# Optimization experiments

Measured on AMD Instinct MI355X. Metric: run time of the kernel, lower is better.

The kernel has to match this reference:

```python
import jax, jax.numpy as jnp
import numpy as np

VOCAB = 100
EMB = 256
HID = 256
B = 8
S = 2048


def setup_inputs() -> dict:
    key = jax.random.key(0)
    ks = jax.random.split(key, 12)
    s_e = 1.0 / np.sqrt(EMB)
    s_h = 1.0 / np.sqrt(HID)
    return {
        "x": jax.random.randint(ks[0], (B, S), 0, VOCAB),
        "embedding": jax.random.normal(ks[1], (VOCAB, EMB), jnp.float32),
        "w_ih": jax.random.uniform(ks[2], (3 * HID, EMB), jnp.float32, -s_e, s_e),
        "w_hh": jax.random.uniform(ks[3], (3 * HID, HID), jnp.float32, -s_h, s_h),
        "b_ih": jax.random.uniform(ks[4], (3 * HID,), jnp.float32, -s_h, s_h),
        "b_hh": jax.random.uniform(ks[5], (3 * HID,), jnp.float32, -s_h, s_h),
        "attn_w": jax.random.uniform(ks[6], (HID, HID), jnp.float32, -s_h, s_h),
        "attn_b": jax.random.uniform(ks[7], (HID,), jnp.float32, -s_h, s_h),
        "comb_w": jax.random.uniform(ks[8], (HID, 2 * HID), jnp.float32, -s_h, s_h),
        "comb_b": jax.random.uniform(ks[9], (HID,), jnp.float32, -s_h, s_h),
        "fc_w": jax.random.uniform(ks[10], (VOCAB, HID), jnp.float32, -s_h, s_h),
        "fc_b": jax.random.uniform(ks[11], (VOCAB,), jnp.float32, -s_h, s_h),
    }


def _gru(emb, w_ih, w_hh, b_ih, b_hh):
    # emb: [B, S, E]; PyTorch GRU gate order: r, z, n
    xg = jnp.einsum('bse,ge->bsg', emb, w_ih) + b_ih  # [B, S, 3H]
    h0 = jnp.zeros((emb.shape[0], HID), emb.dtype)

    def step(h, xg_t):
        hg = h @ w_hh.T + b_hh
        xr, xz, xn = jnp.split(xg_t, 3, axis=-1)
        hr, hz, hn = jnp.split(hg, 3, axis=-1)
        r = jax.nn.sigmoid(xr + hr)
        z = jax.nn.sigmoid(xz + hz)
        n = jnp.tanh(xn + r * hn)
        h_new = (1.0 - z) * n + z * h
        return h_new, h_new

    h_last, hs = jax.lax.scan(step, h0, jnp.swapaxes(xg, 0, 1))
    return jnp.swapaxes(hs, 0, 1), h_last  # [B,S,H], [B,H]


def reference(x, embedding, w_ih, w_hh, b_ih, b_hh, attn_w, attn_b, comb_w, comb_b, fc_w, fc_b):
    emb = embedding[x]  # [B, S, E]
    all_h, h_last = _gru(emb, w_ih, w_hh, b_ih, b_hh)
    keys = jnp.einsum('bsh,kh->bsk', all_h, attn_w) + attn_b  # [B,S,H]
    scores = jnp.einsum('bqh,bkh->bqk', all_h, keys)  # [B,S,S]
    seq = all_h.shape[1]
    causal = jnp.tril(jnp.ones((seq, seq), bool))
    scores = jnp.where(causal[None], scores, -jnp.inf)
    attn = jax.nn.softmax(scores, axis=-1)
    context = jnp.einsum('bqk,bkh->bqh', attn, all_h)  # [B,S,H]
    combined = jnp.concatenate([all_h, context], axis=-1)
    combined = jnp.tanh(jnp.einsum('bsd,hd->bsh', combined, comb_w) + comb_b)
    output = jnp.einsum('bsh,vh->bsv', combined, fc_w) + fc_b
    return output, h_last[None]  # hidden: [num_layers=1, B, H]
```

## Files before the change

kernel.cpp:

```cpp
#include <hip/hip_runtime.h>

#define SEQ  2048
#define NB   8
#define HD   256
#define G3   768
#define NV   100
#define KVB  32

typedef float f32x4 __attribute__((ext_vector_type(4)));
typedef int   i32x4 __attribute__((ext_vector_type(4)));
typedef short s16x8 __attribute__((ext_vector_type(8)));
typedef unsigned short u16x4 __attribute__((ext_vector_type(4)));

#define INV26 1.490116119384765625e-8f

__device__ __forceinline__ float rcp_fast(float x) {
  return __builtin_amdgcn_rcpf(x);
}
__device__ __forceinline__ float sigm(float x) {
  x = fminf(fmaxf(x, -30.f), 30.f);
  return rcp_fast(1.f + __expf(-x));
}
__device__ __forceinline__ float tanh_fast(float x) {
  x = fminf(fmaxf(x, -15.f), 15.f);
  float e = __expf(2.f * x);
  return (e - 1.f) * rcp_fast(e + 1.f);
}
__device__ __forceinline__ void cvt_hilo(float f, unsigned short& h, unsigned short& l) {
  unsigned u = __float_as_uint(f);
  h = (unsigned short)(u >> 16);
  float r = f - __uint_as_float(u & 0xffff0000u);
  l = (unsigned short)(__float_as_uint(r) >> 16);
}

__global__ __launch_bounds__(256) void build_table(
    const float* __restrict__ emb, const float* __restrict__ w_ih,
    const float* __restrict__ b_ih, float* __restrict__ table) {
  __shared__ float eL[256];
  __shared__ float wL[256][37];
  int v = blockIdx.x, tid = threadIdx.x;
  eL[tid] = emb[v * HD + tid];
  for (int gt = 0; gt < 3; ++gt) {
    float acc = b_ih[gt * 256 + tid];
    for (int e0 = 0; e0 < HD; e0 += 32) {
      __syncthreads();
      #pragma unroll
      for (int i = 0; i < 32; ++i) {
        int idx = tid + i * 256;
        int r = idx >> 5, c = idx & 31;
        wL[r][c] = w_ih[(size_t)(gt * 256 + r) * HD + e0 + c];
      }
      __syncthreads();
      #pragma unroll
      for (int c = 0; c < 32; ++c) acc += eL[e0 + c] * wL[tid][c];
    }
    table[((size_t)v * 256 + tid) * 4 + gt] = acc;
  }
}

__global__ void __launch_bounds__(512) gru_scan(
    const int* __restrict__ x, const float* __restrict__ w_hh,
    const float* __restrict__ b_hh, const float* __restrict__ table,
    float* __restrict__ all_h, float* __restrict__ h_last) {
  __shared__ __align__(16) signed char hpk[2][2 * 272];
  __shared__ int xs[SEQ];
  const int b = blockIdx.x;
  int tid = threadIdx.x;
  int lane = tid & 63, wv = tid >> 6;
  int ncol = lane & 15, quad = lane >> 4;
  int usel = quad & 1;
  int j = wv * 32 + usel * 16 + ncol;

  for (int i = tid; i < SEQ; i += 512) xs[i] = x[b * SEQ + i];
  for (int i = tid; i < 2 * 272; i += 512)
    hpk[0][i] = (i >= 272) ? (signed char)-128 : 0;

  i32x4 bw[2][3][4];
  float Cn2[2][3];
  #pragma unroll
  for (int u = 0; u < 2; ++u) {
    #pragma unroll
    for (int t3 = 0; t3 < 3; ++t3) {
      int row = t3 * 256 + wv * 32 + u * 16 + ncol;
      int sw = 0;
      #pragma unroll
      for (int c = 0; c < 4; ++c) {
        const float* p = w_hh + (size_t)row * HD + c * 64 + quad * 16;
        unsigned pw[4] = {0u, 0u, 0u, 0u};
        #pragma unroll
        for (int e = 0; e < 16; ++e) {
          int q = __float2int_rn(p[e] * 2048.f);
          q = max(-127, min(127, q));
          sw += q;
          pw[e >> 2] |= ((unsigned)(q & 255)) << ((e & 3) * 8);
        }
        bw[u][t3][c] = (i32x4){(int)pw[0], (int)pw[1], (int)pw[2], (int)pw[3]};
      }
      sw += __shfl_xor(sw, 16);
      sw += __shfl_xor(sw, 32);
      Cn2[u][t3] = b_hh[row] + 128.f * (float)sw * INV26;
    }
  }
  float Csel[3];
  #pragma unroll
  for (int t3 = 0; t3 < 3; ++t3) Csel[t3] = usel ? Cn2[1][t3] : Cn2[0][t3];

  float hreg = 0.f;
  __syncthreads();
  float xr, xz, xn;
  {
    int v = xs[0];
    f32x4 xg = *(const f32x4*)&table[((size_t)v * 256 + j) * 4];
    xr = xg[0]; xz = xg[1]; xn = xg[2];
  }
  int a_base = (ncol & 1) * 272 + quad * 16;

  for (int t = 0; t < SEQ; ++t) {
    const signed char* cb = hpk[t & 1];
    i32x4 a[4];
    #pragma unroll
    for (int c = 0; c < 4; ++c)
      a[c] = *(const i32x4*)&cb[a_base + c * 64];
    float hg[3];
    #pragma unroll
    for (int t3 = 0; t3 < 3; ++t3) {
      i32x4 A0 = {0, 0, 0, 0}, A1 = {0, 0, 0, 0};
      #pragma unroll
      for (int c = 0; c < 4; ++c) {
        A0 = __builtin_amdgcn_mfma_i32_16x16x64_i8(a[c], bw[0][t3][c], A0, 0, 0, 0);
        A1 = __builtin_amdgcn_mfma_i32_16x16x64_i8(a[c], bw[1][t3][c], A1, 0, 0, 0);
      }
      int d0 = usel ? A1[0] : A0[0];
      int d1 = usel ? A1[1] : A0[1];
      hg[t3] = ((float)d0 * 256.f + (float)d1) * INV26 + Csel[t3];
    }
    float r = sigm(xr + hg[0]);
    float z = sigm(xz + hg[1]);
    float n = tanh_fast(xn + r * hg[2]);
    float h = (1.f - z) * n + z * hreg;
    hreg = h;
    int q = min(__float2int_rn(h * 32768.f), 32767);
    int lou = q & 255;
    int hi8 = (q - lou) >> 8;
    signed char* nx = hpk[(t + 1) & 1];
    if (quad < 2) {
      nx[j] = (signed char)hi8;
      nx[272 + j] = (signed char)(lou - 128);
      all_h[((size_t)b * SEQ + t) * HD + j] = h;
    }
    int v = xs[(t + 1 < SEQ) ? t + 1 : t];
    f32x4 xg = *(const f32x4*)&table[((size_t)v * 256 + j) * 4];
    xr = xg[0]; xz = xg[1]; xn = xg[2];
    __syncthreads();
  }
  if (quad < 2) h_last[b * HD + j] = hreg;
}

template<int ACT>
__global__ __launch_bounds__(256) void gemm_bias(
    const float* __restrict__ A, int lda,
    const float* __restrict__ W, const float* __restrict__ bias,
    float* __restrict__ C, int ldc, int N, int K) {
  __shared__ float As[128][36];
  __shared__ float Ws[64][36];
  int tid = threadIdx.x;
  int m0 = blockIdx.y * 128, n0 = blockIdx.x * 64;
  int ml = tid & 31, g = tid >> 5;
  float acc[4][8];
  #pragma unroll
  for (int i = 0; i < 4; ++i)
    #pragma unroll
    for (int jj = 0; jj < 8; ++jj) acc[i][jj] = 0.f;
  for (int k0 = 0; k0 < K; k0 += 32) {
    __syncthreads();
    #pragma unroll
    for (int i = 0; i < 4; ++i) {
      int idx = tid + i * 256;
      int r = idx >> 3, c4 = (idx & 7) * 4;
      *(f32x4*)&As[r][c4] = *(const f32x4*)&A[(size_t)(m0 + r) * lda + k0 + c4];
    }
    #pragma unroll
    for (int i = 0; i < 2; ++i) {
      int idx = tid + i * 256;
      int r = idx >> 3, c4 = (idx & 7) * 4;
      f32x4 wv = {0.f, 0.f, 0.f, 0.f};
      if (n0 + r < N) wv = *(const f32x4*)&W[(size_t)(n0 + r) * K + k0 + c4];
      *(f32x4*)&Ws[r][c4] = wv;
    }
    __syncthreads();
    #pragma unroll
    for (int k4 = 0; k4 < 32; k4 += 4) {
      f32x4 av[4], wv8[8];
      #pragma unroll
      for (int i = 0; i < 4; ++i) av[i] = *(const f32x4*)&As[ml + i * 32][k4];
      #pragma unroll
      for (int jj = 0; jj < 8; ++jj) wv8[jj] = *(const f32x4*)&Ws[g * 8 + jj][k4];
      #pragma unroll
      for (int kk = 0; kk < 4; ++kk)
        #pragma unroll
        for (int i = 0; i < 4; ++i)
          #pragma unroll
          for (int jj = 0; jj < 8; ++jj)
            acc[i][jj] += av[i][kk] * wv8[jj][kk];
    }
  }
  #pragma unroll
  for (int i = 0; i < 4; ++i) {
    int m = m0 + ml + i * 32;
    #pragma unroll
    for (int jj = 0; jj < 8; ++jj) {
      int n = n0 + g * 8 + jj;
      if (n < N) {
        float val = acc[i][jj] + bias[n];
        if (ACT) val = tanh_fast(val);
        C[(size_t)m * ldc + n] = val;
      }
    }
  }
}

__global__ __launch_bounds__(256) void gemm_keys_pack(
    const float* __restrict__ A,
    const float* __restrict__ W, const float* __restrict__ bias,
    unsigned short* __restrict__ KP) {
  __shared__ float As[128][36];
  __shared__ float Ws[64][36];
  const int K = 256;
  int tid = threadIdx.x;
  int m0 = blockIdx.y * 128, n0 = blockIdx.x * 64;
  int ml = tid & 31, gq = tid >> 5;
  float acc[4][8];
  #pragma unroll
  for (int i = 0; i < 4; ++i)
    #pragma unroll
    for (int jj = 0; jj < 8; ++jj) acc[i][jj] = 0.f;
  for (int k0 = 0; k0 < K; k0 += 32) {
    __syncthreads();
    #pragma unroll
    for (int i = 0; i < 4; ++i) {
      int idx = tid + i * 256;
      int r = idx >> 3, c4 = (idx & 7) * 4;
      *(f32x4*)&As[r][c4] = *(const f32x4*)&A[(size_t)(m0 + r) * HD + k0 + c4];
    }
    #pragma unroll
    for (int i = 0; i < 2; ++i) {
      int idx = tid + i * 256;
      int r = idx >> 3, c4 = (idx & 7) * 4;
      *(f32x4*)&Ws[r][c4] = *(const f32x4*)&W[(size_t)(n0 + r) * K + k0 + c4];
    }
    __syncthreads();
    #pragma unroll
    for (int k4 = 0; k4 < 32; k4 += 4) {
      f32x4 av[4], wv8[8];
      #pragma unroll
      for (int i = 0; i < 4; ++i) av[i] = *(const f32x4*)&As[ml + i * 32][k4];
      #pragma unroll
      for (int jj = 0; jj < 8; ++jj) wv8[jj] = *(const f32x4*)&Ws[gq * 8 + jj][k4];
      #pragma unroll
      for (int kk = 0; kk < 4; ++kk)
        #pragma unroll
        for (int i = 0; i < 4; ++i)
          #pragma unroll
          for (int jj = 0; jj < 8; ++jj)
            acc[i][jj] += av[i][kk] * wv8[jj][kk];
    }
  }
  #pragma unroll
  for (int i = 0; i < 4; ++i) {
    int m = m0 + ml + i * 32;
    int bb = m >> 11, key = m & 2047;
    int kt = key >> 5, g = (key >> 4) & 1, lmk = key & 15;
    int nb = n0 + gq * 8;
    int ch = nb >> 5, kq = (nb >> 3) & 3;
    size_t base = ((size_t)(bb * 64 + kt) * 32 + (g * 8 + ch) * 2) * 512
                + (size_t)(lmk + kq * 16) * 8;
    union { s16x8 v; unsigned short u[8]; } uh, ul;
    #pragma unroll
    for (int jj = 0; jj < 8; ++jj) {
      float val = acc[i][jj] + bias[nb + jj];
      cvt_hilo(val, uh.u[jj], ul.u[jj]);
    }
    *(s16x8*)&KP[base] = uh.v;
    *(s16x8*)&KP[base + 512] = ul.v;
  }
}

__global__ __launch_bounds__(256) void gemm_bias_cat(
    const float* __restrict__ A1, const float* __restrict__ A2,
    const float* __restrict__ W, const float* __restrict__ bias,
    float* __restrict__ C) {
  __shared__ float As[128][36];
  __shared__ float Ws[64][36];
  const int K = 512;
  int tid = threadIdx.x;
  int m0 = blockIdx.y * 128, n0 = blockIdx.x * 64;
  int ml = tid & 31, g = tid >> 5;
  float acc[4][8];
  #pragma unroll
  for (int i = 0; i < 4; ++i)
    #pragma unroll
    for (int jj = 0; jj < 8; ++jj) acc[i][jj] = 0.f;
  for (int k0 = 0; k0 < K; k0 += 32) {
    const float* src = (k0 < 256) ? A1 : A2;
    int kb = (k0 < 256) ? k0 : k0 - 256;
    __syncthreads();
    #pragma unroll
    for (int i = 0; i < 4; ++i) {
      int idx = tid + i * 256;
      int r = idx >> 3, c4 = (idx & 7) * 4;
      *(f32x4*)&As[r][c4] = *(const f32x4*)&src[(size_t)(m0 + r) * 256 + kb + c4];
    }
    #pragma unroll
    for (int i = 0; i < 2; ++i) {
      int idx = tid + i * 256;
      int r = idx >> 3, c4 = (idx & 7) * 4;
      *(f32x4*)&Ws[r][c4] = *(const f32x4*)&W[(size_t)(n0 + r) * K + k0 + c4];
    }
    __syncthreads();
    #pragma unroll
    for (int k4 = 0; k4 < 32; k4 += 4) {
      f32x4 av[4], wv8[8];
      #pragma unroll
      for (int i = 0; i < 4; ++i) av[i] = *(const f32x4*)&As[ml + i * 32][k4];
      #pragma unroll
      for (int jj = 0; jj < 8; ++jj) wv8[jj] = *(const f32x4*)&Ws[g * 8 + jj][k4];
      #pragma unroll
      for (int kk = 0; kk < 4; ++kk)
        #pragma unroll
        for (int i = 0; i < 4; ++i)
          #pragma unroll
          for (int jj = 0; jj < 8; ++jj)
            acc[i][jj] += av[i][kk] * wv8[jj][kk];
    }
  }
  #pragma unroll
  for (int i = 0; i < 4; ++i) {
    int m = m0 + ml + i * 32;
    #pragma unroll
    for (int jj = 0; jj < 8; ++jj) {
      int n = n0 + g * 8 + jj;
      C[(size_t)m * 256 + n] = tanh_fast(acc[i][jj] + bias[n]);
    }
  }
}

__global__ __launch_bounds__(256, 1) void attention_kernel(
    const float* __restrict__ all_h, const unsigned short* __restrict__ kp,
    float* __restrict__ ctxg) {
  __shared__ __align__(16) unsigned short KU[32 * 512];
  __shared__ __align__(16) unsigned short VH[16][524], VL[16][524];
  __shared__ __align__(16) unsigned short PB[4][2][520];
  const int b = blockIdx.y, qb = blockIdx.x;
  int tid = threadIdx.x, lane = tid & 63, wv = tid >> 6;
  int lm = lane & 15, kg = lane >> 4;
  const float* hb = all_h + (size_t)b * SEQ * HD;
  const unsigned short* kpb = kp + (size_t)b * 64 * 16384;
  const int q0 = qb * 64 + wv * 16;

  s16x8 Qh[8], Ql[8];
  {
    const float* qp = hb + (size_t)(q0 + lm) * HD;
    #pragma unroll
    for (int ch = 0; ch < 8; ++ch) {
      union { s16x8 v; unsigned short u[8]; } uh, ul;
      f32x4 a0 = *(const f32x4*)&qp[ch * 32 + kg * 8];
      f32x4 a1 = *(const f32x4*)&qp[ch * 32 + kg * 8 + 4];
      #pragma unroll
      for (int e = 0; e < 4; ++e) {
        cvt_hilo(a0[e], uh.u[e], ul.u[e]);
        cvt_hilo(a1[e], uh.u[4 + e], ul.u[4 + e]);
      }
      Qh[ch] = uh.v; Ql[ch] = ul.v;
    }
  }

  f32x4 co[16];
  #pragma unroll
  for (int ht = 0; ht < 16; ++ht) co[ht] = (f32x4){0.f, 0.f, 0.f, 0.f};
  float mo[4] = {-3e38f, -3e38f, -3e38f, -3e38f};
  float lr[4] = {0.f, 0.f, 0.f, 0.f};

  const int nkt = 2 * qb + 2;
  s16x8 kp8[8];
  f32x4 vreg[8];
  {
    #pragma unroll
    for (int i = 0; i < 8; ++i) {
      int up = wv + i * 4;
      kp8[i] = *(const s16x8*)&kpb[(size_t)up * 512 + lane * 8];
    }
    #pragma unroll
    for (int i = 0; i < 8; ++i) {
      int idx = tid + i * 256;
      int r = idx >> 6, c = idx & 63;
      vreg[i] = *(const f32x4*)&hb[(size_t)r * HD + c * 4];
    }
  }
  for (int kt = 0; kt < nkt; ++kt) {
    __syncthreads();
    #pragma unroll
    for (int i = 0; i < 8; ++i) {
      int up = wv + i * 4;
      *(s16x8*)&KU[up * 512 + lane * 8] = kp8[i];
    }
    #pragma unroll
    for (int i = 0; i < 8; ++i) {
      int idx = tid + i * 256;
      int r = idx >> 6, c = idx & 63;
      f32x4 vv = vreg[i];
      int kgv = r >> 3, ev = r & 7, ht = c >> 2;
      #pragma unroll
      for (int e = 0; e < 4; ++e) {
        unsigned short h16, l16;
        cvt_hilo(vv[e], h16, l16);
        int o = (kgv * 16 + (c & 3) * 4 + e) * 8 + ev;
        VH[ht][o] = h16; VL[ht][o] = l16;
      }
    }
    __syncthreads();
    if (kt + 1 < nkt) {
      const unsigned short* tb = kpb + (size_t)(kt + 1) * 16384;
      #pragma unroll
      for (int i = 0; i < 8; ++i) {
        int up = wv + i * 4;
        kp8[i] = *(const s16x8*)&tb[(size_t)up * 512 + lane * 8];
      }
      int k1 = (kt + 1) * KVB;
      #pragma unroll
      for (int i = 0; i < 8; ++i) {
        int idx = tid + i * 256;
        int r = idx >> 6, c = idx & 63;
        vreg[i] = *(const f32x4*)&hb[(size_t)(k1 + r) * HD + c * 4];
      }
    }
    int k0 = kt * KVB;

    float s[4][2];
    #pragma unroll
    for (int g = 0; g < 2; ++g) {
      f32x4 a0 = {0.f,0.f,0.f,0.f}, a1 = {0.f,0.f,0.f,0.f}, a2 = {0.f,0.f,0.f,0.f};
      #pragma unroll
      for (int ch = 0; ch < 8; ++ch) {
        const unsigned short* ub = &KU[((g * 8 + ch) * 2) * 512 + lane * 8];
        s16x8 bh = *(const s16x8*)ub;
        s16x8 bl = *(const s16x8*)(ub + 512);
        a0 = __builtin_amdgcn_mfma_f32_16x16x32_bf16(Qh[ch], bh, a0, 0, 0, 0);
        a1 = __builtin_amdgcn_mfma_f32_16x16x32_bf16(Ql[ch], bh, a1, 0, 0, 0);
        a2 = __builtin_amdgcn_mfma_f32_16x16x32_bf16(Qh[ch], bl, a2, 0, 0, 0);
      }
      #pragma unroll
      for (int r = 0; r < 4; ++r) s[r][g] = a0[r] + a1[r] + a2[r];
    }
    float p[4][2], al[4];
    #pragma unroll
    for (int r = 0; r < 4; ++r) {
      int qrow = q0 + kg * 4 + r;
      int va = (k0 + lm) <= qrow, vb = (k0 + 16 + lm) <= qrow;
      float ta = va ? s[r][0] : -3e38f;
      float tb = vb ? s[r][1] : -3e38f;
      float t = fmaxf(ta, tb);
      t = fmaxf(t, __shfl_xor(t, 1));
      t = fmaxf(t, __shfl_xor(t, 2));
      t = fmaxf(t, __shfl_xor(t, 4));
      t = fmaxf(t, __shfl_xor(t, 8));
      float mn = fmaxf(mo[r], t);
      al[r] = __expf(mo[r] - mn);
      float pa = va ? __expf(s[r][0] - mn) : 0.f;
      float pb = vb ? __expf(s[r][1] - mn) : 0.f;
      p[r][0] = pa; p[r][1] = pb;
      float rs = pa + pb;
      rs += __shfl_xor(rs, 1);
      rs += __shfl_xor(rs, 2);
      rs += __shfl_xor(rs, 4);
      rs += __shfl_xor(rs, 8);
      lr[r] = lr[r] * al[r] + rs;
      mo[r] = mn;
    }
    #pragma unroll
    for (int r = 0; r < 4; ++r)
      #pragma unroll
      for (int g = 0; g < 2; ++g) {
        unsigned short ph, pl;
        cvt_hilo(p[r][g], ph, pl);
        int key = g * 16 + lm;
        int o = ((key >> 3) * 16 + kg * 4 + r) * 8 + (key & 7);
        PB[wv][0][o] = ph;
        PB[wv][1][o] = pl;
      }
    s16x8 pah = *(const s16x8*)&PB[wv][0][lane * 8];
    s16x8 pal = *(const s16x8*)&PB[wv][1][lane * 8];
    #pragma unroll
    for (int ht = 0; ht < 16; ++ht) {
      f32x4 c = co[ht];
      #pragma unroll
      for (int r = 0; r < 4; ++r) c[r] *= al[r];
      s16x8 vh = *(const s16x8*)&VH[ht][lane * 8];
      s16x8 vl = *(const s16x8*)&VL[ht][lane * 8];
      c = __builtin_amdgcn_mfma_f32_16x16x32_bf16(pah, vh, c, 0, 0, 0);
      c = __builtin_amdgcn_mfma_f32_16x16x32_bf16(pah, vl, c, 0, 0, 0);
      c = __builtin_amdgcn_mfma_f32_16x16x32_bf16(pal, vh, c, 0, 0, 0);
      co[ht] = c;
    }
  }
  float li[4];
  #pragma unroll
  for (int r = 0; r < 4; ++r) li[r] = rcp_fast(lr[r]);
  #pragma unroll
  for (int ht = 0; ht < 16; ++ht)
    #pragma unroll
    for (int r = 0; r < 4; ++r)
      ctxg[((size_t)b * SEQ + q0 + kg * 4 + r) * HD + ht * 16 + lm] = co[ht][r] * li[r];
}

extern "C" void kernel_launch(void* const* d_in, const int* in_sizes, int n_in,
                              void* d_out, int out_size, void* d_ws, size_t ws_size,
                              hipStream_t stream) {
  (void)in_sizes; (void)n_in; (void)out_size; (void)ws_size;
  const int*   x      = (const int*)  d_in[0];
  const float* emb    = (const float*)d_in[1];
  const float* w_ih   = (const float*)d_in[2];
  const float* w_hh   = (const float*)d_in[3];
  const float* b_ih   = (const float*)d_in[4];
  const float* b_hh   = (const float*)d_in[5];
  const float* attn_w = (const float*)d_in[6];
  const float* attn_b = (const float*)d_in[7];
  const float* comb_w = (const float*)d_in[8];
  const float* comb_b = (const float*)d_in[9];
  const float* fc_w   = (const float*)d_in[10];
  const float* fc_b   = (const float*)d_in[11];
  float* out = (float*)d_out;

  float* ws    = (float*)d_ws;
  float* table = ws;
  float* all_h = table + 102400;
  float* keysb = all_h + 4194304;
  float* ctx   = keysb + 4194304;
  float* hlast = out + (size_t)NB * SEQ * NV;
  unsigned short* kpack = (unsigned short*)keysb;

  build_table<<<100, 256, 0, stream>>>(emb, w_ih, b_ih, table);
  gru_scan<<<NB, 512, 0, stream>>>(x, w_hh, b_hh, table, all_h, hlast);
  gemm_keys_pack<<<dim3(4, 128), 256, 0, stream>>>(all_h, attn_w, attn_b, kpack);
  attention_kernel<<<dim3(32, 8), 256, 0, stream>>>(all_h, kpack, ctx);
  gemm_bias_cat<<<dim3(4, 128), 256, 0, stream>>>(all_h, ctx, comb_w, comb_b, keysb);
  gemm_bias<0><<<dim3(2, 128), 256, 0, stream>>>(keysb, 256, fc_w, fc_b, out, 100, 100, 256);
}
```

Measured before the change: 1.880 ms.

## Pre-pack V into split-bf16 MFMA layout in a separate kernel

Adds a pack_v kernel that converts all_h into hi/lo bf16 tiles laid out for the MFMA B operand, once per key tile. The attention kernel now loads these packed tiles directly into LDS instead of converting fp32 V to split bf16 and scattering it every iteration. Since each V tile is reused by many query blocks, this removes repeated conversion work and scattered 16-bit LDS stores. The cost is an extra kernel launch plus extra workspace writes and reads, and it relies on the workspace being large enough for the additional buffer.

```diff
diff --git a/kernel.cpp b/kernel.cpp
--- a/kernel.cpp
+++ b/kernel.cpp
@@ -10,7 +10,6 @@
 typedef float f32x4 __attribute__((ext_vector_type(4)));
 typedef int   i32x4 __attribute__((ext_vector_type(4)));
 typedef short s16x8 __attribute__((ext_vector_type(8)));
-typedef unsigned short u16x4 __attribute__((ext_vector_type(4)));
 
 #define INV26 1.490116119384765625e-8f
 
@@ -285,76 +284,46 @@
   }
 }
 
-__global__ __launch_bounds__(256) void gemm_bias_cat(
-    const float* __restrict__ A1, const float* __restrict__ A2,
-    const float* __restrict__ W, const float* __restrict__ bias,
-    float* __restrict__ C) {
-  __shared__ float As[128][36];
-  __shared__ float Ws[64][36];
-  const int K = 512;
-  int tid = threadIdx.x;
-  int m0 = blockIdx.y * 128, n0 = blockIdx.x * 64;
-  int ml = tid & 31, g = tid >> 5;
-  float acc[4][8];
-  #pragma unroll
-  for (int i = 0; i < 4; ++i)
-    #pragma unroll
-    for (int jj = 0; jj < 8; ++jj) acc[i][jj] = 0.f;
-  for (int k0 = 0; k0 < K; k0 += 32) {
-    const float* src = (k0 < 256) ? A1 : A2;
-    int kb = (k0 < 256) ? k0 : k0 - 256;
-    __syncthreads();
-    #pragma unroll
-    for (int i = 0; i < 4; ++i) {
-      int idx = tid + i * 256;
-      int r = idx >> 3, c4 = (idx & 7) * 4;
-      *(f32x4*)&As[r][c4] = *(const f32x4*)&src[(size_t)(m0 + r) * 256 + kb + c4];
-    }
-    #pragma unroll
-    for (int i = 0; i < 2; ++i) {
-      int idx = tid + i * 256;
-      int r = idx >> 3, c4 = (idx & 7) * 4;
-      *(f32x4*)&Ws[r][c4] = *(const f32x4*)&W[(size_t)(n0 + r) * K + k0 + c4];
-    }
-    __syncthreads();
-    #pragma unroll
-    for (int k4 = 0; k4 < 32; k4 += 4) {
-      f32x4 av[4], wv8[8];
-      #pragma unroll
-      for (int i = 0; i < 4; ++i) av[i] = *(const f32x4*)&As[ml + i * 32][k4];
-      #pragma unroll
-      for (int jj = 0; jj < 8; ++jj) wv8[jj] = *(const f32x4*)&Ws[g * 8 + jj][k4];
-      #pragma unroll
-      for (int kk = 0; kk < 4; ++kk)
-        #pragma unroll
-        for (int i = 0; i < 4; ++i)
-          #pragma unroll
-          for (int jj = 0; jj < 8; ++jj)
-            acc[i][jj] += av[i][kk] * wv8[jj][kk];
-    }
-  }
+__global__ __launch_bounds__(256) void pack_v(
+    const float* __restrict__ all_h, unsigned short* __restrict__ vp) {
+  __shared__ float Lt[32][264];
+  int b = blockIdx.y, kt = blockIdx.x, tid = threadIdx.x;
+  const float* hb = all_h + (size_t)b * SEQ * HD + (size_t)kt * KVB * HD;
+  #pragma unroll
+  for (int i = 0; i < 8; ++i) {
+    int idx = tid + i * 256;
+    int r = idx >> 6, c = idx & 63;
+    *(f32x4*)&Lt[r][c * 4] = *(const f32x4*)&hb[(size_t)r * HD + c * 4];
+  }
+  __syncthreads();
+  unsigned short* vpt = vp + (size_t)(b * 64 + kt) * 16384;
   #pragma unroll
   for (int i = 0; i < 4; ++i) {
-    int m = m0 + ml + i * 32;
-    #pragma unroll
-    for (int jj = 0; jj < 8; ++jj) {
-      int n = n0 + g * 8 + jj;
-      C[(size_t)m * 256 + n] = tanh_fast(acc[i][jj] + bias[n]);
-    }
+    int chunk = tid + i * 256;
+    int ht = chunk >> 6, l = chunk & 63;
+    union { s16x8 v; unsigned short u[8]; } uh, ul;
+    #pragma unroll
+    for (int e = 0; e < 8; ++e) {
+      float f = Lt[(l >> 4) * 8 + e][ht * 16 + (l & 15)];
+      cvt_hilo(f, uh.u[e], ul.u[e]);
+    }
+    *(s16x8*)&vpt[(size_t)(ht * 2) * 512 + l * 8] = uh.v;
+    *(s16x8*)&vpt[(size_t)(ht * 2 + 1) * 512 + l * 8] = ul.v;
   }
 }
 
 __global__ __launch_bounds__(256, 1) void attention_kernel(
     const float* __restrict__ all_h, const unsigned short* __restrict__ kp,
-    float* __restrict__ ctxg) {
+    const unsigned short* __restrict__ vp, float* __restrict__ ctxg) {
   __shared__ __align__(16) unsigned short KU[32 * 512];
-  __shared__ __align__(16) unsigned short VH[16][524], VL[16][524];
+  __shared__ __align__(16) unsigned short VU[32 * 512];
   __shared__ __align__(16) unsigned short PB[4][2][520];
   const int b = blockIdx.y, qb = blockIdx.x;
   int tid = threadIdx.x, lane = tid & 63, wv = tid >> 6;
   int lm = lane & 15, kg = lane >> 4;
   const float* hb = all_h + (size_t)b * SEQ * HD;
   const unsigned short* kpb = kp + (size_t)b * 64 * 16384;
+  const unsigned short* vpb = vp + (size_t)b * 64 * 16384;
   const int q0 = qb * 64 + wv * 16;
 
   s16x8 Qh[8], Ql[8];
@@ -381,20 +350,12 @@
   float lr[4] = {0.f, 0.f, 0.f, 0.f};
 
   const int nkt = 2 * qb + 2;
-  s16x8 kp8[8];
-  f32x4 vreg[8];
-  {
-    #pragma unroll
-    for (int i = 0; i < 8; ++i) {
-      int up = wv + i * 4;
-      kp8[i] = *(const s16x8*)&kpb[(size_t)up * 512 + lane * 8];
-    }
-    #pragma unroll
-    for (int i = 0; i < 8; ++i) {
-      int idx = tid + i * 256;
-      int r = idx >> 6, c = idx & 63;
-      vreg[i] = *(const f32x4*)&hb[(size_t)r * HD + c * 4];
-    }
+  s16x8 kp8[8], vp8[8];
+  #pragma unroll
+  for (int i = 0; i < 8; ++i) {
+    int up = wv + i * 4;
+    kp8[i] = *(const s16x8*)&kpb[(size_t)up * 512 + lane * 8];
+    vp8[i] = *(const s16x8*)&vpb[(size_t)up * 512 + lane * 8];
   }
   for (int kt = 0; kt < nkt; ++kt) {
     __syncthreads();
@@ -402,35 +363,17 @@
     for (int i = 0; i < 8; ++i) {
       int up = wv + i * 4;
       *(s16x8*)&KU[up * 512 + lane * 8] = kp8[i];
-    }
-    #pragma unroll
-    for (int i = 0; i < 8; ++i) {
-      int idx = tid + i * 256;
-      int r = idx >> 6, c = idx & 63;
-      f32x4 vv = vreg[i];
-      int kgv = r >> 3, ev = r & 7, ht = c >> 2;
-      #pragma unroll
-      for (int e = 0; e < 4; ++e) {
-        unsigned short h16, l16;
-        cvt_hilo(vv[e], h16, l16);
-        int o = (kgv * 16 + (c & 3) * 4 + e) * 8 + ev;
-        VH[ht][o] = h16; VL[ht][o] = l16;
-      }
+      *(s16x8*)&VU[up * 512 + lane * 8] = vp8[i];
     }
     __syncthreads();
     if (kt + 1 < nkt) {
-      const unsigned short* tb = kpb + (size_t)(kt + 1) * 16384;
+      const unsigned short* tk = kpb + (size_t)(kt + 1) * 16384;
+      const unsigned short* tv = vpb + (size_t)(kt + 1) * 16384;
       #pragma unroll
       for (int i = 0; i < 8; ++i) {
         int up = wv + i * 4;
-        kp8[i] = *(const s16x8*)&tb[(size_t)up * 512 + lane * 8];
-      }
-      int k1 = (kt + 1) * KVB;
-      #pragma unroll
-      for (int i = 0; i < 8; ++i) {
-        int idx = tid + i * 256;
-        int r = idx >> 6, c = idx & 63;
-        vreg[i] = *(const f32x4*)&hb[(size_t)(k1 + r) * HD + c * 4];
+        kp8[i] = *(const s16x8*)&tk[(size_t)up * 512 + lane * 8];
+        vp8[i] = *(const s16x8*)&tv[(size_t)up * 512 + lane * 8];
       }
     }
     int k0 = kt * KVB;
@@ -494,8 +437,9 @@
       f32x4 c = co[ht];
       #pragma unroll
       for (int r = 0; r < 4; ++r) c[r] *= al[r];
-      s16x8 vh = *(const s16x8*)&VH[ht][lane * 8];
-      s16x8 vl = *(const s16x8*)&VL[ht][lane * 8];
+      const unsigned short* vb2 = &VU[(ht * 2) * 512 + lane * 8];
+      s16x8 vh = *(const s16x8*)vb2;
+      s16x8 vl = *(const s16x8*)(vb2 + 512);
       c = __builtin_amdgcn_mfma_f32_16x16x32_bf16(pah, vh, c, 0, 0, 0);
       c = __builtin_amdgcn_mfma_f32_16x16x32_bf16(pah, vl, c, 0, 0, 0);
       c = __builtin_amdgcn_mfma_f32_16x16x32_bf16(pal, vh, c, 0, 0, 0);
@@ -510,6 +454,65 @@
     #pragma unroll
     for (int r = 0; r < 4; ++r)
       ctxg[((size_t)b * SEQ + q0 + kg * 4 + r) * HD + ht * 16 + lm] = co[ht][r] * li[r];
+}
+
+__global__ __launch_bounds__(256) void gemm_bias_cat(
+    const float* __restrict__ A1, const float* __restrict__ A2,
+    const float* __restrict__ W, const float* __restrict__ bias,
+    float* __restrict__ C) {
+  __shared__ float As[128][36];
+  __shared__ float Ws[64][36];
+  const int K = 512;
+  int tid = threadIdx.x;
+  int m0 = blockIdx.y * 128, n0 = blockIdx.x * 64;
+  int ml = tid & 31, g = tid >> 5;
+  float acc[4][8];
+  #pragma unroll
+  for (int i = 0; i < 4; ++i)
+    #pragma unroll
+    for (int jj = 0; jj < 8; ++jj) acc[i][jj] = 0.f;
+  for (int k0 = 0; k0 < K; k0 += 32) {
+    const float* src = (k0 < 256) ? A1 : A2;
+    int kb = (k0 < 256) ? k0 : k0 - 256;
+    __syncthreads();
+    #pragma unroll
+    for (int i = 0; i < 4; ++i) {
+      int idx = tid + i * 256;
+      int r = idx >> 3, c4 = (idx & 7) * 4;
+      *(f32x4*)&As[r][c4] = *(const f32x4*)&src[(size_t)(m0 + r) * 256 + kb + c4];
+    }
+    #pragma unroll
+    for (int i = 0; i < 2; ++i) {
+      int idx = tid + i * 256;
+      int r = idx >> 3, c4 = (idx & 7) * 4;
+      *(f32x4*)&Ws[r][c4] = *(const f32x4*)&W[(size_t)(n0 + r) * K + k0 + c4];
+    }
+    __syncthreads();
+    #pragma unroll
+    for (int k4 = 0; k4 < 32; k4 += 4) {
+      f32x4 av[4], wv8[8];
+      #pragma unroll
+      for (int i = 0; i < 4; ++i) av[i] = *(const f32x4*)&As[ml + i * 32][k4];
+      #pragma unroll
+      for (int jj = 0; jj < 8; ++jj) wv8[jj] = *(const f32x4*)&Ws[g * 8 + jj][k4];
+      #pragma unroll
+      for (int kk = 0; kk < 4; ++kk)
+        #pragma unroll
+        for (int i = 0; i < 4; ++i)
+          #pragma unroll
+          for (int jj = 0; jj < 8; ++jj)
+            acc[i][jj] += av[i][kk] * wv8[jj][kk];
+    }
+  }
+  #pragma unroll
+  for (int i = 0; i < 4; ++i) {
+    int m = m0 + ml + i * 32;
+    #pragma unroll
+    for (int jj = 0; jj < 8; ++jj) {
+      int n = n0 + g * 8 + jj;
+      C[(size_t)m * 256 + n] = tanh_fast(acc[i][jj] + bias[n]);
+    }
+  }
 }
 
 extern "C" void kernel_launch(void* const* d_in, const int* in_sizes, int n_in,
@@ -535,13 +538,16 @@
   float* all_h = table + 102400;
   float* keysb = all_h + 4194304;
   float* ctx   = keysb + 4194304;
+  float* vbuf  = ctx + 4194304;
   float* hlast = out + (size_t)NB * SEQ * NV;
   unsigned short* kpack = (unsigned short*)keysb;
+  unsigned short* vpack = (unsigned short*)vbuf;
 
   build_table<<<100, 256, 0, stream>>>(emb, w_ih, b_ih, table);
   gru_scan<<<NB, 512, 0, stream>>>(x, w_hh, b_hh, table, all_h, hlast);
   gemm_keys_pack<<<dim3(4, 128), 256, 0, stream>>>(all_h, attn_w, attn_b, kpack);
-  attention_kernel<<<dim3(32, 8), 256, 0, stream>>>(all_h, kpack, ctx);
+  pack_v<<<dim3(64, NB), 256, 0, stream>>>(all_h, vpack);
+  attention_kernel<<<dim3(32, NB), 256, 0, stream>>>(all_h, kpack, vpack, ctx);
   gemm_bias_cat<<<dim3(4, 128), 256, 0, stream>>>(all_h, ctx, comb_w, comb_b, keysb);
   gemm_bias<0><<<dim3(2, 128), 256, 0, stream>>>(keysb, 256, fc_w, fc_b, out, 100, 100, 256);
 }
```

After: 1.850 ms, median of 2. About the same (-1.6%).
